# Performance work log

Hardware: AMD Instinct MI355X
Metric: run time of the kernel (lower is better)

Reference implementation:

```python
import jax, jax.numpy as jnp
import numpy as np

EMB = 1024
HEADS = 16
HEAD_DIM = EMB // HEADS
DFF = 4 * EMB
EPS = 1e-5


def gelu_tanh(x):
    c = jnp.sqrt(jnp.asarray(2.0 / jnp.pi, dtype=x.dtype))
    return 0.5 * x * (1.0 + jnp.tanh(c * (x + 0.044715 * x ** 3)))


def layernorm(x, scale, shift):
    mean = jnp.mean(x, axis=-1, keepdims=True)
    var = jnp.mean((x - mean) ** 2, axis=-1, keepdims=True)
    return scale * ((x - mean) / jnp.sqrt(var + EPS)) + shift


def setup_inputs() -> dict:
    key = jax.random.key(0)
    ks = jax.random.split(key, 12)
    s = 0.02
    return {
        "x": jax.random.normal(ks[0], (2, 2048, EMB), dtype=jnp.float32),
        "Wq": jax.random.normal(ks[1], (EMB, EMB), dtype=jnp.float32) * s,
        "Wk": jax.random.normal(ks[2], (EMB, EMB), dtype=jnp.float32) * s,
        "Wv": jax.random.normal(ks[3], (EMB, EMB), dtype=jnp.float32) * s,
        "Wo": jax.random.normal(ks[4], (EMB, EMB), dtype=jnp.float32) * s,
        "bo": jnp.zeros((EMB,), dtype=jnp.float32),
        "W1": jax.random.normal(ks[5], (EMB, DFF), dtype=jnp.float32) * s,
        "b1": jnp.zeros((DFF,), dtype=jnp.float32),
        "W2": jax.random.normal(ks[6], (DFF, EMB), dtype=jnp.float32) * s,
        "b2": jnp.zeros((EMB,), dtype=jnp.float32),
        "g1": jnp.ones((EMB,), dtype=jnp.float32),
        "s1": jnp.zeros((EMB,), dtype=jnp.float32),
        "g2": jnp.ones((EMB,), dtype=jnp.float32),
        "s2": jnp.zeros((EMB,), dtype=jnp.float32),
    }


def reference(x, Wq, Wk, Wv, Wo, bo, W1, b1, W2, b2, g1, s1, g2, s2):
    B, S, E = x.shape
    # attention sub-block (pre-norm, residual)
    h = layernorm(x, g1, s1)
    Q = (h @ Wq).reshape(B, S, HEADS, HEAD_DIM)
    K = (h @ Wk).reshape(B, S, HEADS, HEAD_DIM)
    V = (h @ Wv).reshape(B, S, HEADS, HEAD_DIM)
    # scores: [B, H, S, S]
    scores = jnp.einsum("bqhd,bkhd->bhqk", Q, K)
    causal = jnp.tril(jnp.ones((S, S), dtype=bool))
    scores = jnp.where(causal, scores, -jnp.inf)
    attn = jax.nn.softmax(scores / np.sqrt(HEAD_DIM), axis=-1)
    ctx = jnp.einsum("bhqk,bkhd->bqhd", attn, V).reshape(B, S, E)
    x = x + (ctx @ Wo + bo)
    # FFN sub-block
    h = layernorm(x, g2, s2)
    h = gelu_tanh(h @ W1 + b1) @ W2 + b2
    return x + h
```

## Files before the change

### kernel.cpp

```cpp
#include <hip/hip_runtime.h>
#include <hip/hip_bf16.h>

typedef __attribute__((ext_vector_type(8))) short short8;
typedef __attribute__((ext_vector_type(4))) float f32x4;

#define EMB   1024
#define DFF   4096
#define S_LEN 2048
#define NB    2
#define MTOT  (NB * S_LEN)
#define HEADS 16
#define HDIM  64
#define QKVN  3072
#define BK    32

__device__ __forceinline__ float bf2f(unsigned short u) {
  return __uint_as_float(((unsigned int)u) << 16);
}
__device__ __forceinline__ unsigned short f2bf(float f) {
  unsigned int x = __float_as_uint(f);
  unsigned int r = (x + 0x7fffu + ((x >> 16) & 1u)) >> 16;
  return (unsigned short)r;
}
__device__ __forceinline__ unsigned int cvtpk(float a, float b) {
  unsigned int r;
  asm("v_cvt_pk_bf16_f32 %0, %1, %2" : "=v"(r) : "v"(a), "v"(b));
  return r;
}

__device__ __forceinline__ void gl_lds16(const unsigned short* g, unsigned short* l) {
  __builtin_amdgcn_global_load_lds(
      (const __attribute__((address_space(1))) unsigned int*)g,
      (__attribute__((address_space(3))) unsigned int*)l, 16, 0, 0);
}

__global__ __launch_bounds__(256) void fused_transpose(
    const float* __restrict__ Wq, const float* __restrict__ Wk,
    const float* __restrict__ Wv, const float* __restrict__ Wo,
    const float* __restrict__ W1, const float* __restrict__ W2,
    unsigned short* __restrict__ wtQ, unsigned short* __restrict__ wtK,
    unsigned short* __restrict__ wtV, unsigned short* __restrict__ wtO,
    unsigned short* __restrict__ wtW1, unsigned short* __restrict__ wtW2)
{
  __shared__ float t[32][33];
  const int bid = (int)blockIdx.x;
  const float* W; unsigned short* Wt; int K, N, local;
  if (bid < 4096) {
    const int sel = bid >> 10; local = bid & 1023; K = 1024; N = 1024;
    W  = sel == 0 ? Wq  : sel == 1 ? Wk  : sel == 2 ? Wv  : Wo;
    Wt = sel == 0 ? wtQ : sel == 1 ? wtK : sel == 2 ? wtV : wtO;
  } else if (bid < 8192) {
    local = bid - 4096; K = 1024; N = 4096; W = W1; Wt = wtW1;
  } else {
    local = bid - 8192; K = 4096; N = 1024; W = W2; Wt = wtW2;
  }
  const int nbx = N >> 5;
  const int n0 = (local % nbx) * 32, k0 = (local / nbx) * 32;
  const int tx = threadIdx.x, ty = threadIdx.y;
#pragma unroll
  for (int i = 0; i < 4; ++i) {
    int r = ty + i * 8;
    t[r][tx] = W[(size_t)(k0 + r) * N + n0 + tx];
  }
  __syncthreads();
#pragma unroll
  for (int i = 0; i < 4; ++i) {
    int r = ty + i * 8;
    Wt[(size_t)(n0 + r) * K + k0 + tx] = f2bf(t[tx][r]);
  }
}

__global__ __launch_bounds__(256) void transpose_v(
    const unsigned short* __restrict__ qkv, unsigned short* __restrict__ Vt)
{
  __shared__ unsigned short t[32][33];
  const int s0 = blockIdx.x * 32, d0 = blockIdx.y * 32, bh = blockIdx.z;
  const int b = bh >> 4, h = bh & 15;
  const int tx = threadIdx.x, ty = threadIdx.y;
#pragma unroll
  for (int i = 0; i < 4; ++i) {
    int r = ty + i * 8;
    t[r][tx] = qkv[((size_t)(b * S_LEN + s0 + r)) * QKVN + 2048 + h * HDIM + d0 + tx];
  }
  __syncthreads();
#pragma unroll
  for (int i = 0; i < 4; ++i) {
    int r = ty + i * 8;
    Vt[((size_t)bh * HDIM + d0 + r) * S_LEN + s0 + tx] = t[tx][r];
  }
}

__global__ __launch_bounds__(256) void ln_kernel(
    const float* __restrict__ X, const float* __restrict__ g,
    const float* __restrict__ sh, unsigned short* __restrict__ H)
{
  const int row = blockIdx.x, t = threadIdx.x;
  const float* xr = X + (size_t)row * EMB;
  float4 v = *(const float4*)(xr + t * 4);
  float s  = v.x + v.y + v.z + v.w;
  float ss = v.x * v.x + v.y * v.y + v.z * v.z + v.w * v.w;
#pragma unroll
  for (int off = 32; off > 0; off >>= 1) {
    s  += __shfl_xor(s, off);
    ss += __shfl_xor(ss, off);
  }
  __shared__ float rs[4], rss[4];
  const int wid = t >> 6;
  if ((t & 63) == 0) { rs[wid] = s; rss[wid] = ss; }
  __syncthreads();
  s  = rs[0] + rs[1] + rs[2] + rs[3];
  ss = rss[0] + rss[1] + rss[2] + rss[3];
  const float mean = s * (1.f / EMB);
  const float var  = ss * (1.f / EMB) - mean * mean;
  const float rstd = rsqrtf(var + 1e-5f);
  float4 gv = *(const float4*)(g + t * 4);
  float4 sv = *(const float4*)(sh + t * 4);
  ushort4 o;
  o.x = f2bf((v.x - mean) * rstd * gv.x + sv.x);
  o.y = f2bf((v.y - mean) * rstd * gv.y + sv.y);
  o.z = f2bf((v.z - mean) * rstd * gv.z + sv.z);
  o.w = f2bf((v.w - mean) * rstd * gv.w + sv.w);
  *(ushort4*)(H + (size_t)row * EMB + t * 4) = o;
}

__device__ __forceinline__ float gelu_tanh_f(float v) {
  float u = v + 0.044715f * v * v * v;
  float t = tanhf(0.7978845608028654f * u);
  return 0.5f * v * (1.0f + t);
}

template <int MODE, int BN>
__global__ __launch_bounds__(256, 2) void gemm_gl(
    const unsigned short* __restrict__ A, const unsigned short* __restrict__ Bt,
    int M, int N, int Kloop, int Kld, int nbx,
    const float* __restrict__ bias, const float* __restrict__ resf,
    float* __restrict__ outf, unsigned short* __restrict__ outb)
{
  constexpr int NFRAG = BN / 32;
  __shared__ unsigned short As[2][128 * BK];
  __shared__ unsigned short Bs[2][BN * BK];

  const int tid = threadIdx.x;
  const int lane = tid & 63, wid = tid >> 6;
  const int nwg = (int)gridDim.x;
  const int cpx = nwg >> 3;
  const int bid = (int)blockIdx.x;
  const int swz = (bid & 7) * cpx + (bid >> 3);
  const int by = swz / nbx;
  const int bx = swz - by * nbx;
  const int m0 = by * 128, n0 = bx * BN;
  const int wr = wid >> 1, wc = wid & 1;
  const int l16 = lane & 15, kg = lane >> 4;

  const int sr  = lane >> 2;
  const int scs = (((lane & 3) ^ ((lane >> 3) & 3))) * 8;
  const int xr = (l16 >> 1) & 3;

  const unsigned short* Abase = A + (size_t)m0 * Kld;
  const unsigned short* Bbase = Bt + (size_t)n0 * Kld;

  f32x4 acc[4][NFRAG];
#pragma unroll
  for (int i = 0; i < 4; ++i)
#pragma unroll
    for (int j = 0; j < NFRAG; ++j) acc[i][j] = (f32x4){0.f, 0.f, 0.f, 0.f};

  const int nt = Kloop / BK;

#define STAGE(buf, t)                                                          \
  do {                                                                         \
    const int k0_ = (t) * BK;                                                  \
    _Pragma("unroll")                                                          \
    for (int i_ = 0; i_ < 2; ++i_) {                                           \
      const int chunk_ = wid * 2 + i_;                                         \
      gl_lds16(Abase + (size_t)(chunk_ * 16 + sr) * Kld + k0_ + scs,           \
               &As[buf][0] + chunk_ * 512);                                    \
    }                                                                          \
    _Pragma("unroll")                                                          \
    for (int i_ = 0; i_ < BN / 64; ++i_) {                                     \
      const int chunk_ = wid * (BN / 64) + i_;                                 \
      gl_lds16(Bbase + (size_t)(chunk_ * 16 + sr) * Kld + k0_ + scs,           \
               &Bs[buf][0] + chunk_ * 512);                                    \
    }                                                                          \
  } while (0)

  STAGE(0, 0);
  STAGE(1, 1);
  if constexpr (BN == 128) asm volatile("s_waitcnt vmcnt(4)" ::: "memory");
  else                     asm volatile("s_waitcnt vmcnt(3)" ::: "memory");
  __builtin_amdgcn_s_barrier();

  int b = 0;
  for (int t = 0; t < nt; ++t) {
    short8 af[4], bfr[NFRAG];
#pragma unroll
    for (int i = 0; i < 4; ++i)
      af[i] = *(const short8*)(&As[b][(wr * 64 + i * 16 + l16) * BK + (kg ^ xr) * 8]);
#pragma unroll
    for (int j = 0; j < NFRAG; ++j)
      bfr[j] = *(const short8*)(&Bs[b][(wc * (BN / 2) + j * 16 + l16) * BK + (kg ^ xr) * 8]);
#pragma unroll
    for (int i = 0; i < 4; ++i)
#pragma unroll
      for (int j = 0; j < NFRAG; ++j)
        acc[i][j] = __builtin_amdgcn_mfma_f32_16x16x32_bf16(af[i], bfr[j], acc[i][j], 0, 0, 0);
    asm volatile("s_waitcnt lgkmcnt(0)" ::: "memory");
    __builtin_amdgcn_s_barrier();
    if (t + 2 < nt) {
      STAGE(b, t + 2);
      if constexpr (BN == 128) asm volatile("s_waitcnt vmcnt(4)" ::: "memory");
      else                     asm volatile("s_waitcnt vmcnt(3)" ::: "memory");
    } else {
      asm volatile("s_waitcnt vmcnt(0)" ::: "memory");
    }
    __builtin_amdgcn_s_barrier();
    b ^= 1;
  }
#undef STAGE

#pragma unroll
  for (int i = 0; i < 4; ++i) {
#pragma unroll
    for (int j = 0; j < NFRAG; ++j) {
      const int c = n0 + wc * (BN / 2) + j * 16 + l16;
#pragma unroll
      for (int r = 0; r < 4; ++r) {
        const int row = m0 + wr * 64 + i * 16 + kg * 4 + r;
        const size_t idx = (size_t)row * N + c;
        float v = acc[i][j][r];
        if constexpr (MODE == 0) {
          outb[idx] = f2bf(c < 1024 ? v * 0.18033688011112042f : v);
        } else if constexpr (MODE == 1) {
          outf[idx] = v + bias[c] + resf[idx];
        } else if constexpr (MODE == 2) {
          outb[idx] = f2bf(gelu_tanh_f(v + bias[c]));
        } else if constexpr (MODE == 4) {
          outb[idx] = f2bf(v);
        } else {
          outf[idx] = v + bias[c] + resf[idx] + bf2f(outb[idx]);
        }
      }
    }
  }
}

__global__ __launch_bounds__(256) void attn_mfma(
    const unsigned short* __restrict__ qkv, const unsigned short* __restrict__ Vt,
    unsigned short* __restrict__ ctx)
{
  __shared__ unsigned short Ks[64][64];
  __shared__ unsigned short Vs[64][64];
  __shared__ unsigned short Ps[4][2][16][64];

  const int tid  = threadIdx.x;
  const int lane = tid & 63, wv = tid >> 6;
  const int l16  = lane & 15, kg = lane >> 4;
  const int bid  = (int)blockIdx.x;
  const int swz  = (bid & 7) * 64 + (bid >> 3);
  const int pair = swz & 15;
  const int bh   = swz >> 4;
  const int b    = bh >> 4, h = bh & 15;
  const int qtg0 = pair;
  const int qtg1 = 31 - pair;

  const size_t qbase  = ((size_t)b * S_LEN) * QKVN + h * HDIM;
  const size_t kbase  = qbase + 1024;
  const size_t vtbase = ((size_t)bh * HDIM) * S_LEN;
  const size_t cbase  = ((size_t)b * S_LEN) * EMB + h * HDIM;

  short8 qf[2][2];
#pragma unroll
  for (int g = 0; g < 2; ++g) {
    const int qt = g ? qtg1 : qtg0;
    const unsigned short* qrow =
        qkv + qbase + (size_t)(qt * 64 + wv * 16 + l16) * QKVN;
    qf[g][0] = *(const short8*)(qrow + kg * 8);
    qf[g][1] = *(const short8*)(qrow + 32 + kg * 8);
  }

  f32x4 o[2][4];
#pragma unroll
  for (int g = 0; g < 2; ++g)
#pragma unroll
    for (int dt = 0; dt < 4; ++dt) o[g][dt] = (f32x4){0.f, 0.f, 0.f, 0.f};
  float m[2] = {-1e30f, -1e30f}, l[2] = {0.f, 0.f};

  const int srow = tid >> 2;
  const int c0   = tid & 3;
  const int sx   = srow & 7;
  const int col0 = ((2 * c0)     ^ sx) * 8;
  const int col1 = ((2 * c0 + 1) ^ sx) * 8;
  const int rx   = l16 & 7;
  const int ntiles = qtg1 + 1;

  const unsigned short* ksrc = qkv + kbase + (size_t)srow * QKVN + c0 * 16;
  const unsigned short* vsrc = Vt + vtbase + (size_t)srow * S_LEN + c0 * 16;
  short8 k0 = *(const short8*)(ksrc);
  short8 k1 = *(const short8*)(ksrc + 8);
  short8 v0 = *(const short8*)(vsrc);
  short8 v1 = *(const short8*)(vsrc + 8);

  for (int kt = 0; kt < ntiles; ++kt) {
    __syncthreads();
    *(short8*)(&Ks[srow][col0]) = k0;
    *(short8*)(&Ks[srow][col1]) = k1;
    *(short8*)(&Vs[srow][col0]) = v0;
    *(short8*)(&Vs[srow][col1]) = v1;
    __syncthreads();

    if (kt + 1 < ntiles) {
      const unsigned short* kn =
          qkv + kbase + (size_t)((kt + 1) * 64 + srow) * QKVN + c0 * 16;
      const unsigned short* vn =
          Vt + vtbase + (size_t)srow * S_LEN + (kt + 1) * 64 + c0 * 16;
      k0 = *(const short8*)(kn);
      k1 = *(const short8*)(kn + 8);
      v0 = *(const short8*)(vn);
      v1 = *(const short8*)(vn + 8);
    }

    const bool act0 = (kt <= qtg0);

    short8 kf0[4], kf1[4];
#pragma unroll
    for (int j = 0; j < 4; ++j) {
      kf0[j] = *(const short8*)(&Ks[j * 16 + l16][(kg ^ rx) * 8]);
      kf1[j] = *(const short8*)(&Ks[j * 16 + l16][((kg + 4) ^ rx) * 8]);
    }

    float fac[2] = {1.f, 1.f};
    bool resc[2] = {false, false};
#pragma unroll
    for (int g = 0; g < 2; ++g) {
      if (g == 0 && !act0) continue;
      const int qt = g ? qtg1 : qtg0;

      f32x4 sa[4];
      __builtin_amdgcn_s_setprio(1);
#pragma unroll
      for (int j = 0; j < 4; ++j) {
        sa[j] = (f32x4){0.f, 0.f, 0.f, 0.f};
        sa[j] = __builtin_amdgcn_mfma_f32_16x16x32_bf16(kf0[j], qf[g][0], sa[j], 0, 0, 0);
        sa[j] = __builtin_amdgcn_mfma_f32_16x16x32_bf16(kf1[j], qf[g][1], sa[j], 0, 0, 0);
      }
      __builtin_amdgcn_s_setprio(0);

      if (kt == qt) {
        const int qloc = wv * 16 + l16;
#pragma unroll
        for (int j = 0; j < 4; ++j)
#pragma unroll
          for (int r = 0; r < 4; ++r)
            if (j * 16 + kg * 4 + r > qloc) sa[j][r] = -1e30f;
      }

      float m0j = fmaxf(fmaxf(sa[0][0], sa[0][1]), fmaxf(sa[0][2], sa[0][3]));
      float m1j = fmaxf(fmaxf(sa[1][0], sa[1][1]), fmaxf(sa[1][2], sa[1][3]));
      float m2j = fmaxf(fmaxf(sa[2][0], sa[2][1]), fmaxf(sa[2][2], sa[2][3]));
      float m3j = fmaxf(fmaxf(sa[3][0], sa[3][1]), fmaxf(sa[3][2], sa[3][3]));
      float mx = fmaxf(fmaxf(m0j, m1j), fmaxf(m2j, m3j));
      mx = fmaxf(mx, __shfl_xor(mx, 16));
      mx = fmaxf(mx, __shfl_xor(mx, 32));
      if (!__all(mx - m[g] <= 8.0f)) {
        const float mn = fmaxf(m[g], mx);
        fac[g] = exp2f(m[g] - mn);
        m[g] = mn;
        resc[g] = true;
      }
      const float mcur = m[g];
      float ps = 0.f;
#pragma unroll
      for (int j = 0; j < 4; ++j) {
        float p0 = exp2f(sa[j][0] - mcur);
        float p1 = exp2f(sa[j][1] - mcur);
        float p2 = exp2f(sa[j][2] - mcur);
        float p3 = exp2f(sa[j][3] - mcur);
        sa[j][0] = p0; sa[j][1] = p1; sa[j][2] = p2; sa[j][3] = p3;
        ps += (p0 + p1) + (p2 + p3);
      }
      ps += __shfl_xor(ps, 16);
      ps += __shfl_xor(ps, 32);
      l[g] = l[g] * fac[g] + ps;

#pragma unroll
      for (int j = 0; j < 4; ++j) {
        uint2 pw;
        pw.x = cvtpk(sa[j][0], sa[j][1]);
        pw.y = cvtpk(sa[j][2], sa[j][3]);
        *(uint2*)(&Ps[wv][g][l16][((2 * j + (kg >> 1)) ^ rx) * 8 + (kg & 1) * 4]) = pw;
      }
    }

#pragma unroll
    for (int g = 0; g < 2; ++g) {
      if (resc[g]) {
#pragma unroll
        for (int dt = 0; dt < 4; ++dt)
#pragma unroll
          for (int r = 0; r < 4; ++r) o[g][dt][r] *= fac[g];
      }
    }

    short8 pf[2][2];
#pragma unroll
    for (int g = 0; g < 2; ++g) {
      if (g == 0 && !act0) continue;
      pf[g][0] = *(const short8*)(&Ps[wv][g][l16][(kg ^ rx) * 8]);
      pf[g][1] = *(const short8*)(&Ps[wv][g][l16][((kg + 4) ^ rx) * 8]);
    }
    __builtin_amdgcn_s_setprio(1);
#pragma unroll
    for (int dt = 0; dt < 4; ++dt) {
      short8 vf0 = *(const short8*)(&Vs[dt * 16 + l16][(kg ^ rx) * 8]);
      short8 vf1 = *(const short8*)(&Vs[dt * 16 + l16][((kg + 4) ^ rx) * 8]);
#pragma unroll
      for (int g = 0; g < 2; ++g) {
        if (g == 0 && !act0) continue;
        o[g][dt] = __builtin_amdgcn_mfma_f32_16x16x32_bf16(vf0, pf[g][0], o[g][dt], 0, 0, 0);
        o[g][dt] = __builtin_amdgcn_mfma_f32_16x16x32_bf16(vf1, pf[g][1], o[g][dt], 0, 0, 0);
      }
    }
    __builtin_amdgcn_s_setprio(0);
  }

#pragma unroll
  for (int g = 0; g < 2; ++g) {
    const int qt = g ? qtg1 : qtg0;
    const float inv = 1.0f / l[g];
    const int qrow = qt * 64 + wv * 16 + l16;
#pragma unroll
    for (int dt = 0; dt < 4; ++dt) {
      uint2 cw;
      cw.x = cvtpk(o[g][dt][0] * inv, o[g][dt][1] * inv);
      cw.y = cvtpk(o[g][dt][2] * inv, o[g][dt][3] * inv);
      *(uint2*)(&ctx[cbase + (size_t)qrow * EMB + dt * 16 + kg * 4]) = cw;
    }
  }
}

extern "C" void kernel_launch(void* const* d_in, const int* in_sizes, int n_in,
                              void* d_out, int out_size, void* d_ws, size_t ws_size,
                              hipStream_t stream)
{
  const float* x  = (const float*)d_in[0];
  const float* Wq = (const float*)d_in[1];
  const float* Wk = (const float*)d_in[2];
  const float* Wv = (const float*)d_in[3];
  const float* Wo = (const float*)d_in[4];
  const float* bo = (const float*)d_in[5];
  const float* W1 = (const float*)d_in[6];
  const float* b1 = (const float*)d_in[7];
  const float* W2 = (const float*)d_in[8];
  const float* b2 = (const float*)d_in[9];
  const float* g1 = (const float*)d_in[10];
  const float* s1 = (const float*)d_in[11];
  const float* g2 = (const float*)d_in[12];
  const float* s2 = (const float*)d_in[13];

  float* out = (float*)d_out;
  char* ws = (char*)d_ws;
  const size_t MB = 1024 * 1024;
  unsigned short* wtQ  = (unsigned short*)(ws + 0 * MB);
  unsigned short* wtK  = (unsigned short*)(ws + 2 * MB);
  unsigned short* wtV  = (unsigned short*)(ws + 4 * MB);
  unsigned short* wtO  = (unsigned short*)(ws + 6 * MB);
  unsigned short* wtW1 = (unsigned short*)(ws + 8 * MB);
  unsigned short* wtW2 = (unsigned short*)(ws + 16 * MB);
  unsigned short* h    = (unsigned short*)(ws + 24 * MB);
  unsigned short* qkv  = (unsigned short*)(ws + 32 * MB);
  unsigned short* Vt   = (unsigned short*)(ws + 56 * MB);
  unsigned short* ctxb = h;
  unsigned short* h2   = h;
  unsigned short* pbuf = h;
  unsigned short* gbuf = qkv;

  fused_transpose<<<dim3(12288), dim3(32, 8), 0, stream>>>(
      Wq, Wk, Wv, Wo, W1, W2, wtQ, wtK, wtV, wtO, wtW1, wtW2);

  ln_kernel<<<MTOT, 256, 0, stream>>>(x, g1, s1, h);

  gemm_gl<0, 128><<<dim3(24 * 32), 256, 0, stream>>>(
      h, wtQ, MTOT, QKVN, 1024, 1024, 24, nullptr, nullptr, nullptr, qkv);

  transpose_v<<<dim3(64, 2, 32), dim3(32, 8), 0, stream>>>(qkv, Vt);

  attn_mfma<<<dim3(512), 256, 0, stream>>>(qkv, Vt, ctxb);

  gemm_gl<1, 64><<<dim3(16 * 32), 256, 0, stream>>>(
      ctxb, wtO, MTOT, 1024, 1024, 1024, 16, bo, x, out, nullptr);

  ln_kernel<<<MTOT, 256, 0, stream>>>(out, g2, s2, h2);

  gemm_gl<2, 128><<<dim3(32 * 32), 256, 0, stream>>>(
      h2, wtW1, MTOT, DFF, 1024, 1024, 32, b1, nullptr, nullptr, gbuf);

  gemm_gl<4, 64><<<dim3(16 * 32), 256, 0, stream>>>(
      gbuf + 2048, wtW2 + 2048, MTOT, 1024, 2048, DFF, 16, nullptr, nullptr, nullptr, pbuf);
  gemm_gl<5, 64><<<dim3(16 * 32), 256, 0, stream>>>(
      gbuf, wtW2, MTOT, 1024, 2048, DFF, 16, b2, out, out, pbuf);
}
```

Baseline: 263.7 us.

## Fuse V transpose into QKV GEMM epilogue and drop split-K W2 GEMM

```diff
diff --git a/kernel.cpp b/kernel.cpp
--- a/kernel.cpp
+++ b/kernel.cpp
@@ -11,7 +11,7 @@
 #define MTOT  (NB * S_LEN)
 #define HEADS 16
 #define HDIM  64
-#define QKVN  3072
+#define QKN   2048
 #define BK    32
 
 __device__ __forceinline__ float bf2f(unsigned short u) {
@@ -42,51 +42,32 @@
     unsigned short* __restrict__ wtV, unsigned short* __restrict__ wtO,
     unsigned short* __restrict__ wtW1, unsigned short* __restrict__ wtW2)
 {
-  __shared__ float t[32][33];
+  __shared__ float t[64][33];
   const int bid = (int)blockIdx.x;
   const float* W; unsigned short* Wt; int K, N, local;
-  if (bid < 4096) {
-    const int sel = bid >> 10; local = bid & 1023; K = 1024; N = 1024;
+  if (bid < 2048) {
+    const int sel = bid >> 9; local = bid & 511; K = 1024; N = 1024;
     W  = sel == 0 ? Wq  : sel == 1 ? Wk  : sel == 2 ? Wv  : Wo;
     Wt = sel == 0 ? wtQ : sel == 1 ? wtK : sel == 2 ? wtV : wtO;
-  } else if (bid < 8192) {
-    local = bid - 4096; K = 1024; N = 4096; W = W1; Wt = wtW1;
+  } else if (bid < 4096) {
+    local = bid - 2048; K = 1024; N = 4096; W = W1; Wt = wtW1;
   } else {
-    local = bid - 8192; K = 4096; N = 1024; W = W2; Wt = wtW2;
+    local = bid - 4096; K = 4096; N = 1024; W = W2; Wt = wtW2;
   }
   const int nbx = N >> 5;
-  const int n0 = (local % nbx) * 32, k0 = (local / nbx) * 32;
+  const int n0 = (local % nbx) * 32, k0 = (local / nbx) * 64;
   const int tx = threadIdx.x, ty = threadIdx.y;
 #pragma unroll
+  for (int i = 0; i < 8; ++i) {
+    const int kr = i * 8 + ty;
+    t[kr][tx] = W[(size_t)(k0 + kr) * N + n0 + tx];
+  }
+  __syncthreads();
+#pragma unroll
   for (int i = 0; i < 4; ++i) {
-    int r = ty + i * 8;
-    t[r][tx] = W[(size_t)(k0 + r) * N + n0 + tx];
-  }
-  __syncthreads();
-#pragma unroll
-  for (int i = 0; i < 4; ++i) {
-    int r = ty + i * 8;
-    Wt[(size_t)(n0 + r) * K + k0 + tx] = f2bf(t[tx][r]);
-  }
-}
-
-__global__ __launch_bounds__(256) void transpose_v(
-    const unsigned short* __restrict__ qkv, unsigned short* __restrict__ Vt)
-{
-  __shared__ unsigned short t[32][33];
-  const int s0 = blockIdx.x * 32, d0 = blockIdx.y * 32, bh = blockIdx.z;
-  const int b = bh >> 4, h = bh & 15;
-  const int tx = threadIdx.x, ty = threadIdx.y;
-#pragma unroll
-  for (int i = 0; i < 4; ++i) {
-    int r = ty + i * 8;
-    t[r][tx] = qkv[((size_t)(b * S_LEN + s0 + r)) * QKVN + 2048 + h * HDIM + d0 + tx];
-  }
-  __syncthreads();
-#pragma unroll
-  for (int i = 0; i < 4; ++i) {
-    int r = ty + i * 8;
-    Vt[((size_t)bh * HDIM + d0 + r) * S_LEN + s0 + tx] = t[tx][r];
+    const int r = ty + i * 8;
+    const unsigned int u = cvtpk(t[2 * tx][r], t[2 * tx + 1][r]);
+    *(unsigned int*)(&Wt[(size_t)(n0 + r) * K + k0 + 2 * tx]) = u;
   }
 }
 
@@ -134,7 +115,8 @@
     const unsigned short* __restrict__ A, const unsigned short* __restrict__ Bt,
     int M, int N, int Kloop, int Kld, int nbx,
     const float* __restrict__ bias, const float* __restrict__ resf,
-    float* __restrict__ outf, unsigned short* __restrict__ outb)
+    float* __restrict__ outf, unsigned short* __restrict__ outb,
+    unsigned short* __restrict__ vt)
 {
   constexpr int NFRAG = BN / 32;
   __shared__ unsigned short As[2][128 * BK];
@@ -223,21 +205,36 @@
 #pragma unroll
     for (int j = 0; j < NFRAG; ++j) {
       const int c = n0 + wc * (BN / 2) + j * 16 + l16;
-#pragma unroll
-      for (int r = 0; r < 4; ++r) {
-        const int row = m0 + wr * 64 + i * 16 + kg * 4 + r;
-        const size_t idx = (size_t)row * N + c;
-        float v = acc[i][j][r];
-        if constexpr (MODE == 0) {
-          outb[idx] = f2bf(c < 1024 ? v * 0.18033688011112042f : v);
-        } else if constexpr (MODE == 1) {
-          outf[idx] = v + bias[c] + resf[idx];
-        } else if constexpr (MODE == 2) {
-          outb[idx] = f2bf(gelu_tanh_f(v + bias[c]));
-        } else if constexpr (MODE == 4) {
-          outb[idx] = f2bf(v);
+      if constexpr (MODE == 0) {
+        if (c >= 2048) {
+          const int row0 = m0 + wr * 64 + i * 16 + kg * 4;
+          const int dcol = c - 2048;
+          ushort4 w4;
+          w4.x = f2bf(acc[i][j][0]); w4.y = f2bf(acc[i][j][1]);
+          w4.z = f2bf(acc[i][j][2]); w4.w = f2bf(acc[i][j][3]);
+          *(ushort4*)(&vt[((size_t)((row0 >> 11) * 16 + (dcol >> 6)) * 64 +
+                           (dcol & 63)) * 2048 + (row0 & 2047)]) = w4;
         } else {
-          outf[idx] = v + bias[c] + resf[idx] + bf2f(outb[idx]);
+          const float sc = (c < 1024) ? 0.18033688011112042f : 1.0f;
+#pragma unroll
+          for (int r = 0; r < 4; ++r) {
+            const int row = m0 + wr * 64 + i * 16 + kg * 4 + r;
+            outb[(size_t)row * QKN + c] = f2bf(acc[i][j][r] * sc);
+          }
+        }
+      } else {
+#pragma unroll
+        for (int r = 0; r < 4; ++r) {
+          const int row = m0 + wr * 64 + i * 16 + kg * 4 + r;
+          const size_t idx = (size_t)row * N + c;
+          float v = acc[i][j][r];
+          if constexpr (MODE == 1) {
+            outf[idx] = v + bias[c] + resf[idx];
+          } else if constexpr (MODE == 2) {
+            outb[idx] = f2bf(gelu_tanh_f(v + bias[c]));
+          } else {
+            outf[idx] = v + bias[c] + resf[idx];
+          }
         }
       }
     }
@@ -263,7 +260,7 @@
   const int qtg0 = pair;
   const int qtg1 = 31 - pair;
 
-  const size_t qbase  = ((size_t)b * S_LEN) * QKVN + h * HDIM;
+  const size_t qbase  = ((size_t)b * S_LEN) * QKN + h * HDIM;
   const size_t kbase  = qbase + 1024;
   const size_t vtbase = ((size_t)bh * HDIM) * S_LEN;
   const size_t cbase  = ((size_t)b * S_LEN) * EMB + h * HDIM;
@@ -273,7 +270,7 @@
   for (int g = 0; g < 2; ++g) {
     const int qt = g ? qtg1 : qtg0;
     const unsigned short* qrow =
-        qkv + qbase + (size_t)(qt * 64 + wv * 16 + l16) * QKVN;
+        qkv + qbase + (size_t)(qt * 64 + wv * 16 + l16) * QKN;
     qf[g][0] = *(const short8*)(qrow + kg * 8);
     qf[g][1] = *(const short8*)(qrow + 32 + kg * 8);
   }
@@ -293,7 +290,7 @@
   const int rx   = l16 & 7;
   const int ntiles = qtg1 + 1;
 
-  const unsigned short* ksrc = qkv + kbase + (size_t)srow * QKVN + c0 * 16;
+  const unsigned short* ksrc = qkv + kbase + (size_t)srow * QKN + c0 * 16;
   const unsigned short* vsrc = Vt + vtbase + (size_t)srow * S_LEN + c0 * 16;
   short8 k0 = *(const short8*)(ksrc);
   short8 k1 = *(const short8*)(ksrc + 8);
@@ -310,7 +307,7 @@
 
     if (kt + 1 < ntiles) {
       const unsigned short* kn =
-          qkv + kbase + (size_t)((kt + 1) * 64 + srow) * QKVN + c0 * 16;
+          qkv + kbase + (size_t)((kt + 1) * 64 + srow) * QKN + c0 * 16;
       const unsigned short* vn =
           Vt + vtbase + (size_t)srow * S_LEN + (kt + 1) * 64 + c0 * 16;
       k0 = *(const short8*)(kn);
@@ -471,31 +468,26 @@
   unsigned short* Vt   = (unsigned short*)(ws + 56 * MB);
   unsigned short* ctxb = h;
   unsigned short* h2   = h;
-  unsigned short* pbuf = h;
   unsigned short* gbuf = qkv;
 
-  fused_transpose<<<dim3(12288), dim3(32, 8), 0, stream>>>(
+  fused_transpose<<<dim3(6144), dim3(32, 8), 0, stream>>>(
       Wq, Wk, Wv, Wo, W1, W2, wtQ, wtK, wtV, wtO, wtW1, wtW2);
 
   ln_kernel<<<MTOT, 256, 0, stream>>>(x, g1, s1, h);
 
   gemm_gl<0, 128><<<dim3(24 * 32), 256, 0, stream>>>(
-      h, wtQ, MTOT, QKVN, 1024, 1024, 24, nullptr, nullptr, nullptr, qkv);
-
-  transpose_v<<<dim3(64, 2, 32), dim3(32, 8), 0, stream>>>(qkv, Vt);
+      h, wtQ, MTOT, 3072, 1024, 1024, 24, nullptr, nullptr, nullptr, qkv, Vt);
 
   attn_mfma<<<dim3(512), 256, 0, stream>>>(qkv, Vt, ctxb);
 
   gemm_gl<1, 64><<<dim3(16 * 32), 256, 0, stream>>>(
-      ctxb, wtO, MTOT, 1024, 1024, 1024, 16, bo, x, out, nullptr);
+      ctxb, wtO, MTOT, 1024, 1024, 1024, 16, bo, x, out, nullptr, nullptr);
 
   ln_kernel<<<MTOT, 256, 0, stream>>>(out, g2, s2, h2);
 
   gemm_gl<2, 128><<<dim3(32 * 32), 256, 0, stream>>>(
-      h2, wtW1, MTOT, DFF, 1024, 1024, 32, b1, nullptr, nullptr, gbuf);
-
-  gemm_gl<4, 64><<<dim3(16 * 32), 256, 0, stream>>>(
-      gbuf + 2048, wtW2 + 2048, MTOT, 1024, 2048, DFF, 16, nullptr, nullptr, nullptr, pbuf);
-  gemm_gl<5, 64><<<dim3(16 * 32), 256, 0, stream>>>(
-      gbuf, wtW2, MTOT, 1024, 2048, DFF, 16, b2, out, out, pbuf);
-}
+      h2, wtW1, MTOT, DFF, 1024, 1024, 32, b1, nullptr, nullptr, gbuf, nullptr);
+
+  gemm_gl<3, 64><<<dim3(16 * 32), 256, 0, stream>>>(
+      gbuf, wtW2, MTOT, 1024, DFF, DFF, 16, b2, out, out, nullptr, nullptr);
+}
```

After: 256.0 us. 2.9% less time.
